# Optimization experiments

Measured on AMD Instinct MI355X. Metric: run time of the kernel, lower is better.

## Reference

```python
import jax, jax.numpy as jnp
import numpy as np

N = 50000          # node_num
E = 800000         # edges before self-loops (avg degree 16)
H = 1              # heads
C = 64             # out_channel (== embedding dim)
D_IN = 64          # in_channel
NEG_SLOPE = 0.2    # GraphLayer leaky_relu negative_slope
BN_EPS = 1e-5


def setup_inputs() -> dict:
    key = jax.random.key(0)
    ks = jax.random.split(key, 12)
    x = jax.random.normal(ks[0], (N, D_IN), jnp.float32)
    # random edges with no self-loops (forward removes then re-adds self-loops)
    src = jax.random.randint(ks[1], (E,), 0, N, dtype=jnp.int32)
    off = jax.random.randint(ks[2], (E,), 1, N, dtype=jnp.int32)
    dst = (src + off) % N
    edge_index = jnp.stack([src, dst])            # [2, E], row0=j (source), row1=i (target)
    embedding = jax.random.normal(ks[3], (N, C), jnp.float32)
    sc = 1.0 / np.sqrt(D_IN)
    W = jax.random.normal(ks[4], (H * C, D_IN), jnp.float32) * sc   # lin.weight
    att_i = jax.random.normal(ks[5], (1, H, C), jnp.float32) * 0.1
    att_j = jax.random.normal(ks[6], (1, H, C), jnp.float32) * 0.1
    att_em_i = jax.random.normal(ks[7], (1, H, C), jnp.float32) * 0.1
    att_em_j = jax.random.normal(ks[8], (1, H, C), jnp.float32) * 0.1
    bias = jnp.zeros((C,), jnp.float32)           # GraphLayer bias (concat=False)
    bn_gamma = jnp.ones((C,), jnp.float32)
    bn_beta = jnp.zeros((C,), jnp.float32)
    return {"x": x, "edge_index": edge_index, "embedding": embedding, "W": W,
            "att_i": att_i, "att_j": att_j, "att_em_i": att_em_i, "att_em_j": att_em_j,
            "bias": bias, "bn_gamma": bn_gamma, "bn_beta": bn_beta}


def reference(x, edge_index, embedding, W, att_i, att_j, att_em_i, att_em_j, bias, bn_gamma, bn_beta):
    n = x.shape[0]
    xl = (x @ W.T).reshape(n, H, C)                       # lin(x) -> [N, H, C]
    # add self-loops (input edges have none)
    loops = jnp.arange(n, dtype=edge_index.dtype)
    src = jnp.concatenate([edge_index[0], loops])         # j
    dst = jnp.concatenate([edge_index[1], loops])         # i (aggregation target)
    x_j = xl[src]                                         # [E', H, C]
    x_i = xl[dst]
    emb_i = embedding[dst][:, None, :]                    # [E', 1, C] broadcast over heads
    emb_j = embedding[src][:, None, :]
    # alpha = <cat(x_i, emb_i), cat(att_i, att_em_i)> + <cat(x_j, emb_j), cat(att_j, att_em_j)>
    a = ((x_i * att_i).sum(-1) + (emb_i * att_em_i).sum(-1)
         + (x_j * att_j).sum(-1) + (emb_j * att_em_j).sum(-1))   # [E', H]
    a = jnp.where(a >= 0, a, NEG_SLOPE * a)               # leaky_relu(0.2)
    # segment softmax over target nodes
    amax = jax.ops.segment_max(a, dst, num_segments=n)    # every node has a self-loop
    ea = jnp.exp(a - amax[dst])
    denom = jax.ops.segment_sum(ea, dst, num_segments=n)
    alpha = ea / (denom[dst] + 1e-16)                     # [E', H]
    msg = x_j * alpha[..., None]                          # [E', H, C]
    out = jax.ops.segment_sum(msg, dst, num_segments=n)   # [N, H, C]
    out = out.mean(axis=1) + bias                         # concat=False -> head mean
    # BatchNorm1d (training mode: batch stats) + ReLU
    mu = out.mean(axis=0)
    var = ((out - mu) ** 2).mean(axis=0)
    out = (out - mu) * jax.lax.rsqrt(var + BN_EPS) * bn_gamma + bn_beta
    return jnp.maximum(out, 0.0)
```

## Files before the change

kernel.cpp:

```cpp
#include <hip/hip_runtime.h>
#include <hip/hip_bf16.h>

#define NEG_SLOPE 0.2f
#define BN_EPS 1e-5f
#define CAP 48
#define OWNMAX 768

typedef __attribute__((ext_vector_type(8))) short bf16x8;
typedef __attribute__((ext_vector_type(4))) float f32x4;

__device__ __forceinline__ bf16x8 pk8(float4 a, float4 b) {
    union { __hip_bfloat16 h; short s; } u;
    bf16x8 r;
    u.h = __float2bfloat16(a.x); r[0] = u.s;
    u.h = __float2bfloat16(a.y); r[1] = u.s;
    u.h = __float2bfloat16(a.z); r[2] = u.s;
    u.h = __float2bfloat16(a.w); r[3] = u.s;
    u.h = __float2bfloat16(b.x); r[4] = u.s;
    u.h = __float2bfloat16(b.y); r[5] = u.s;
    u.h = __float2bfloat16(b.z); r[6] = u.s;
    u.h = __float2bfloat16(b.w); r[7] = u.s;
    return r;
}

__global__ void __launch_bounds__(256, 8)
k_scatter_mfma(const float* __restrict__ x, const float* __restrict__ W,
               const float* __restrict__ emb,
               const float* __restrict__ att_i, const float* __restrict__ att_j,
               const float* __restrict__ att_em_i, const float* __restrict__ att_em_j,
               const int* __restrict__ src, const int* __restrict__ dst, int E,
               int* __restrict__ cursor, unsigned short* __restrict__ bucket,
               __hip_bfloat16* __restrict__ xlh, float* __restrict__ s_i,
               float* __restrict__ s_j, int N) {
    __shared__ int nown;
    __shared__ unsigned int own[OWNMAX];
    int tid = threadIdx.x;

    int gw = blockIdx.x * 4 + (tid >> 6);
    int ntiles = (N + 15) >> 4;
    int lane = tid & 63;
    int m = lane & 15;
    int q = lane >> 4;
    int r0 = gw * 16;
    int rload = r0 + m; if (rload > N - 1) rload = N - 1;
    const float* xrow = x + (size_t)rload * 64;
    float4 xa0 = *(const float4*)(xrow + q * 8);
    float4 xa1 = *(const float4*)(xrow + q * 8 + 4);
    float4 xb0 = *(const float4*)(xrow + 32 + q * 8);
    float4 xb1 = *(const float4*)(xrow + 32 + q * 8 + 4);

    {
        int myx = blockIdx.x & 7;
        int slice = blockIdx.x >> 3;
        int per = ((E + 255) >> 8);
        per = (per + 3) & ~3;
        int e0 = slice * per;
        int e1 = e0 + per; if (e1 > E) e1 = E;
        if (tid == 0) nown = 0;
        __syncthreads();
        if (e0 < e1) {
            int e1a = e0 + ((e1 - e0) & ~3);
#define APP(dd, ss) if ((((dd) >> 6) & 7) == myx) { \
            int k_ = atomicAdd(&nown, 1); \
            if (k_ < OWNMAX) own[k_] = ((unsigned)(dd) << 16) | (unsigned)(ss); }
            for (int e = e0 + tid * 4; e < e1a; e += 1024) {
                int4 d4 = *(const int4*)(dst + e);
                int4 s4 = *(const int4*)(src + e);
                APP(d4.x, s4.x)
                APP(d4.y, s4.y)
                APP(d4.z, s4.z)
                APP(d4.w, s4.w)
            }
            for (int e = e1a + tid; e < e1; e += 256) {
                int d = dst[e]; int s = src[e];
                APP(d, s)
            }
#undef APP
        }
        __syncthreads();
        int n = nown < OWNMAX ? nown : OWNMAX;
        unsigned pa = (tid < n) ? own[tid] : 0u;
        unsigned pb = (tid + 256 < n) ? own[tid + 256] : 0u;
        if (tid < n) {
            int d = pa >> 16;
            int p = atomicAdd(&cursor[d], 1);
            if (p < CAP) bucket[(size_t)d * CAP + p] = (unsigned short)(pa & 0xffffu);
        }
        if (tid + 256 < n) {
            int d = pb >> 16;
            int p = atomicAdd(&cursor[d], 1);
            if (p < CAP) bucket[(size_t)d * CAP + p] = (unsigned short)(pb & 0xffffu);
        }
        for (int k = tid + 512; k < n; k += 256) {
            unsigned pc = own[k];
            int d = pc >> 16;
            int p = atomicAdd(&cursor[d], 1);
            if (p < CAP) bucket[(size_t)d * CAP + p] = (unsigned short)(pc & 0xffffu);
        }
    }

    if (gw >= ntiles) return;
    bf16x8 A0 = pk8(xa0, xa1);
    bf16x8 A1 = pk8(xb0, xb1);

    f32x4 acc0 = {0.f, 0.f, 0.f, 0.f}, acc1 = acc0, acc2 = acc0, acc3 = acc0;
#define CTILE(ct, accv) { \
        const float* wrow = W + (size_t)(ct * 16 + m) * 64; \
        float4 wb0 = *(const float4*)(wrow + q * 8); \
        float4 wb1 = *(const float4*)(wrow + q * 8 + 4); \
        float4 wb2 = *(const float4*)(wrow + 32 + q * 8); \
        float4 wb3 = *(const float4*)(wrow + 32 + q * 8 + 4); \
        bf16x8 B0 = pk8(wb0, wb1); \
        bf16x8 B1 = pk8(wb2, wb3); \
        accv = __builtin_amdgcn_mfma_f32_16x16x32_bf16(A0, B0, accv, 0, 0, 0); \
        accv = __builtin_amdgcn_mfma_f32_16x16x32_bf16(A1, B1, accv, 0, 0, 0); }
    CTILE(0, acc0) CTILE(1, acc1) CTILE(2, acc2) CTILE(3, acc3)
#undef CTILE

    float ati0 = att_i[m],    ati1 = att_i[16 + m],    ati2 = att_i[32 + m],    ati3 = att_i[48 + m];
    float atj0 = att_j[m],    atj1 = att_j[16 + m],    atj2 = att_j[32 + m],    atj3 = att_j[48 + m];
    float aei0 = att_em_i[m], aei1 = att_em_i[16 + m], aei2 = att_em_i[32 + m], aei3 = att_em_i[48 + m];
    float aej0 = att_em_j[m], aej1 = att_em_j[16 + m], aej2 = att_em_j[32 + m], aej3 = att_em_j[48 + m];
#pragma unroll
    for (int reg = 0; reg < 4; ++reg) {
        int r = r0 + q * 4 + reg;
        if (r < N) {
            float v0 = acc0[reg], v1 = acc1[reg], v2 = acc2[reg], v3 = acc3[reg];
            __hip_bfloat16* xo = xlh + (size_t)r * 64 + m;
            xo[0]  = __float2bfloat16(v0);
            xo[16] = __float2bfloat16(v1);
            xo[32] = __float2bfloat16(v2);
            xo[48] = __float2bfloat16(v3);
            const float* er = emb + (size_t)r * 64 + m;
            float e0 = er[0], e1 = er[16], e2 = er[32], e3 = er[48];
            float pi = v0 * ati0 + v1 * ati1 + v2 * ati2 + v3 * ati3
                     + e0 * aei0 + e1 * aei1 + e2 * aei2 + e3 * aei3;
            float pj = v0 * atj0 + v1 * atj1 + v2 * atj2 + v3 * atj3
                     + e0 * aej0 + e1 * aej1 + e2 * aej2 + e3 * aej3;
#pragma unroll
            for (int o = 1; o < 16; o <<= 1) {
                pi += __shfl_xor(pi, o, 64);
                pj += __shfl_xor(pj, o, 64);
            }
            if (m == 0) { s_i[r] = pi; s_j[r] = pj; }
        }
    }
}

__global__ void __launch_bounds__(256, 8)
k_aggregate(const __hip_bfloat16* __restrict__ xlh, const float* __restrict__ s_i,
            const float* __restrict__ s_j, const int* __restrict__ cursor,
            const unsigned short* __restrict__ bucket, const float* __restrict__ bias,
            __hip_bfloat16* __restrict__ preh, int N) {
    int lane = threadIdx.x & 63;
    int w = threadIdx.x >> 6;
    int blk = blockIdx.x;
    int t = blk >> 3;
    int g = ((t >> 4) << 7) + ((blk & 7) << 4) + (t & 15);
    int i = g * 4 + w;
    if (i >= N) return;

    int deg = cursor[i];
    deg = deg < CAP ? deg : CAP;
    size_t base = (size_t)i * CAP;
    float sii = s_i[i];
    float sji = s_j[i];
    float selfx = (float)xlh[(size_t)i * 64 + lane];
    float bi = bias[lane];
    int jreg = 0;
    if (lane < deg) jreg = (int)bucket[base + lane];
    float wreg = 0.f;
    if (lane < deg) {
        float a = sii + s_j[jreg];
        a = a >= 0.f ? a : NEG_SLOPE * a;
        wreg = __expf(a);
    }
    float a_self = sii + sji;
    a_self = a_self >= 0.f ? a_self : NEG_SLOPE * a_self;
    float w_self = __expf(a_self);
    float dsum = wreg;
#pragma unroll
    for (int o = 32; o; o >>= 1) dsum += __shfl_xor(dsum, o, 64);

    float acc = w_self * selfx;
    int wbits = __float_as_int(wreg);
    int nb = (deg + 15) >> 4;
#define GL(k) int j##k = __builtin_amdgcn_readlane(jreg, e + k); \
              float u##k = __int_as_float(__builtin_amdgcn_readlane(wbits, e + k)); \
              float v##k = (float)xlh[(size_t)j##k * 64 + lane];
#define FM(k) acc = fmaf(u##k, v##k, acc);
    for (int b = 0; b < nb; ++b) {
        int e = b << 4;
        GL(0) GL(1) GL(2) GL(3) GL(4) GL(5) GL(6) GL(7)
        GL(8) GL(9) GL(10) GL(11) GL(12) GL(13) GL(14) GL(15)
        FM(0) FM(1) FM(2) FM(3) FM(4) FM(5) FM(6) FM(7)
        FM(8) FM(9) FM(10) FM(11) FM(12) FM(13) FM(14) FM(15)
    }
#undef GL
#undef FM
    float denom = dsum + w_self + 1e-16f;
    preh[(size_t)i * 64 + lane] = __float2bfloat16(acc / denom + bi);
}

__global__ void k_stats(const __hip_bfloat16* __restrict__ preh, int N,
                        float* __restrict__ sums) {
    int lane = threadIdx.x & 63, w = threadIdx.x >> 6;
    int gwave = blockIdx.x * (blockDim.x >> 6) + w;
    int stride = gridDim.x * (blockDim.x >> 6);
    float s = 0.f, q = 0.f;
    for (int r = gwave; r < N; r += stride) {
        float v = (float)preh[(size_t)r * 64 + lane];
        s += v;
        q = fmaf(v, v, q);
    }
    __shared__ float ls[4][64], lq[4][64];
    ls[w][lane] = s;
    lq[w][lane] = q;
    __syncthreads();
    if (w == 0) {
        s = ls[0][lane] + ls[1][lane] + ls[2][lane] + ls[3][lane];
        q = lq[0][lane] + lq[1][lane] + lq[2][lane] + lq[3][lane];
        atomicAdd(&sums[lane], s);
        atomicAdd(&sums[64 + lane], q);
    }
}

__global__ void __launch_bounds__(256, 4)
k_norm(const __hip_bfloat16* __restrict__ preh, const float* __restrict__ sums,
       const float* __restrict__ gamma, const float* __restrict__ beta,
       float* __restrict__ out, int N, int total4) {
    __shared__ float sc_sh[64], sh_sh[64];
    int tid = threadIdx.x;
    if (tid < 64) {
        float invN = 1.f / (float)N;
        float mu = sums[tid] * invN;
        float var = sums[64 + tid] * invN - mu * mu;
        float sc = gamma[tid] * rsqrtf(var + BN_EPS);
        sc_sh[tid] = sc;
        sh_sh[tid] = beta[tid] - mu * sc;
    }
    __syncthreads();
    typedef __attribute__((ext_vector_type(4))) short s16x4;
    union { s16x4 v; short s[4]; } u;
    for (int i = blockIdx.x * blockDim.x + tid; i < total4; i += gridDim.x * blockDim.x) {
        int c = (i & 15) * 4;
        u.v = ((const s16x4*)preh)[i];
        float4 r;
        union { __hip_bfloat16 h; short s; } cv;
        cv.s = u.s[0]; r.x = fmaxf(fmaf((float)cv.h, sc_sh[c + 0], sh_sh[c + 0]), 0.f);
        cv.s = u.s[1]; r.y = fmaxf(fmaf((float)cv.h, sc_sh[c + 1], sh_sh[c + 1]), 0.f);
        cv.s = u.s[2]; r.z = fmaxf(fmaf((float)cv.h, sc_sh[c + 2], sh_sh[c + 2]), 0.f);
        cv.s = u.s[3]; r.w = fmaxf(fmaf((float)cv.h, sc_sh[c + 3], sh_sh[c + 3]), 0.f);
        ((float4*)out)[i] = r;
    }
}

extern "C" void kernel_launch(void* const* d_in, const int* in_sizes, int n_in,
                              void* d_out, int out_size, void* d_ws, size_t ws_size,
                              hipStream_t stream) {
    const float* x        = (const float*)d_in[0];
    const int*   ei       = (const int*)d_in[1];
    const float* emb      = (const float*)d_in[2];
    const float* W        = (const float*)d_in[3];
    const float* att_i    = (const float*)d_in[4];
    const float* att_j    = (const float*)d_in[5];
    const float* att_em_i = (const float*)d_in[6];
    const float* att_em_j = (const float*)d_in[7];
    const float* bias     = (const float*)d_in[8];
    const float* gamma    = (const float*)d_in[9];
    const float* beta     = (const float*)d_in[10];

    int N = in_sizes[0] / 64;
    int E = in_sizes[1] / 2;
    const int* srcv = ei;
    const int* dstv = ei + E;

    char* ws = (char*)d_ws;
    size_t o = 0;
    auto alloc = [&](size_t bytes) -> char* {
        char* p = ws + o;
        o += bytes;
        o = (o + 255) & ~(size_t)255;
        return p;
    };
    __hip_bfloat16* xlh    = (__hip_bfloat16*)alloc((size_t)N * 64 * 2);
    __hip_bfloat16* preh   = (__hip_bfloat16*)alloc((size_t)N * 64 * 2);
    float* s_i             = (float*)alloc((size_t)N * 4);
    float* s_j             = (float*)alloc((size_t)N * 4);
    unsigned short* bucket = (unsigned short*)alloc((size_t)N * CAP * 2);
    char*  zbase  = alloc((size_t)N * 4 + 128 * 4);
    int*   cursor = (int*)zbase;
    float* sums   = (float*)(zbase + (size_t)N * 4);

    hipMemsetAsync(zbase, 0, (size_t)N * 4 + 128 * 4, stream);

    k_scatter_mfma<<<2048, 256, 0, stream>>>(x, W, emb, att_i, att_j, att_em_i,
                                             att_em_j, srcv, dstv, E, cursor, bucket,
                                             xlh, s_i, s_j, N);
    int nblk2 = (((N + 3) / 4) + 127) & ~127;
    k_aggregate<<<nblk2, 256, 0, stream>>>(xlh, s_i, s_j, cursor, bucket,
                                           bias, preh, N);
    k_stats<<<256, 256, 0, stream>>>(preh, N, sums);
    int total4 = N * 16;
    k_norm<<<512, 256, 0, stream>>>(preh, sums, gamma, beta, (float*)d_out, N, total4);
}
```

Before: 180.0 us.

## Pair edges per wave in aggregation, remap GEMM tiles, add nontemporal loads/stores

The aggregation kernel now splits the wave into two half-waves that each gather a different neighbor row with 32-bit loads of two bf16 channels, then combines the halves with a cross-lane shuffle. This halves the number of serialized gather iterations per node. The fused scatter/GEMM kernel maps GEMM tiles across waves with a 2048-block stride and skips loading x for waves with no tile. Nontemporal hints are added on streaming loads and stores (x, emb, xlh writes, bucket, output) to reduce cache pollution. The changes add shuffle and select overhead, and the GEMM remap assumes a fixed grid size.

```diff
diff --git a/kernel.cpp b/kernel.cpp
--- a/kernel.cpp
+++ b/kernel.cpp
@@ -8,18 +8,19 @@
 
 typedef __attribute__((ext_vector_type(8))) short bf16x8;
 typedef __attribute__((ext_vector_type(4))) float f32x4;
-
-__device__ __forceinline__ bf16x8 pk8(float4 a, float4 b) {
+typedef __attribute__((ext_vector_type(4))) int i32x4;
+
+__device__ __forceinline__ bf16x8 pk8(f32x4 a, f32x4 b) {
     union { __hip_bfloat16 h; short s; } u;
     bf16x8 r;
-    u.h = __float2bfloat16(a.x); r[0] = u.s;
-    u.h = __float2bfloat16(a.y); r[1] = u.s;
-    u.h = __float2bfloat16(a.z); r[2] = u.s;
-    u.h = __float2bfloat16(a.w); r[3] = u.s;
-    u.h = __float2bfloat16(b.x); r[4] = u.s;
-    u.h = __float2bfloat16(b.y); r[5] = u.s;
-    u.h = __float2bfloat16(b.z); r[6] = u.s;
-    u.h = __float2bfloat16(b.w); r[7] = u.s;
+    u.h = __float2bfloat16(a[0]); r[0] = u.s;
+    u.h = __float2bfloat16(a[1]); r[1] = u.s;
+    u.h = __float2bfloat16(a[2]); r[2] = u.s;
+    u.h = __float2bfloat16(a[3]); r[3] = u.s;
+    u.h = __float2bfloat16(b[0]); r[4] = u.s;
+    u.h = __float2bfloat16(b[1]); r[5] = u.s;
+    u.h = __float2bfloat16(b[2]); r[6] = u.s;
+    u.h = __float2bfloat16(b[3]); r[7] = u.s;
     return r;
 }
 
@@ -35,19 +36,23 @@
     __shared__ int nown;
     __shared__ unsigned int own[OWNMAX];
     int tid = threadIdx.x;
-
-    int gw = blockIdx.x * 4 + (tid >> 6);
-    int ntiles = (N + 15) >> 4;
     int lane = tid & 63;
+    int wid = tid >> 6;
     int m = lane & 15;
     int q = lane >> 4;
+
+    int gw = wid * 2048 + (int)blockIdx.x;
+    int ntiles = (N + 15) >> 4;
+    bool hasgemm = gw < ntiles;
     int r0 = gw * 16;
-    int rload = r0 + m; if (rload > N - 1) rload = N - 1;
-    const float* xrow = x + (size_t)rload * 64;
-    float4 xa0 = *(const float4*)(xrow + q * 8);
-    float4 xa1 = *(const float4*)(xrow + q * 8 + 4);
-    float4 xb0 = *(const float4*)(xrow + 32 + q * 8);
-    float4 xb1 = *(const float4*)(xrow + 32 + q * 8 + 4);
+    f32x4 xa0 = {0,0,0,0}, xa1 = xa0, xb0 = xa0, xb1 = xa0;
+    if (hasgemm) {
+        const float* xrow = x + (size_t)(r0 + m) * 64;
+        xa0 = __builtin_nontemporal_load((const f32x4*)(xrow + q * 8));
+        xa1 = __builtin_nontemporal_load((const f32x4*)(xrow + q * 8 + 4));
+        xb0 = __builtin_nontemporal_load((const f32x4*)(xrow + 32 + q * 8));
+        xb1 = __builtin_nontemporal_load((const f32x4*)(xrow + 32 + q * 8 + 4));
+    }
 
     {
         int myx = blockIdx.x & 7;
@@ -64,12 +69,12 @@
             int k_ = atomicAdd(&nown, 1); \
             if (k_ < OWNMAX) own[k_] = ((unsigned)(dd) << 16) | (unsigned)(ss); }
             for (int e = e0 + tid * 4; e < e1a; e += 1024) {
-                int4 d4 = *(const int4*)(dst + e);
-                int4 s4 = *(const int4*)(src + e);
-                APP(d4.x, s4.x)
-                APP(d4.y, s4.y)
-                APP(d4.z, s4.z)
-                APP(d4.w, s4.w)
+                i32x4 d4 = *(const i32x4*)(dst + e);
+                i32x4 s4 = *(const i32x4*)(src + e);
+                APP(d4[0], s4[0])
+                APP(d4[1], s4[1])
+                APP(d4[2], s4[2])
+                APP(d4[3], s4[3])
             }
             for (int e = e1a + tid; e < e1; e += 256) {
                 int d = dst[e]; int s = src[e];
@@ -99,17 +104,17 @@
         }
     }
 
-    if (gw >= ntiles) return;
+    if (!hasgemm) return;
     bf16x8 A0 = pk8(xa0, xa1);
     bf16x8 A1 = pk8(xb0, xb1);
 
     f32x4 acc0 = {0.f, 0.f, 0.f, 0.f}, acc1 = acc0, acc2 = acc0, acc3 = acc0;
 #define CTILE(ct, accv) { \
         const float* wrow = W + (size_t)(ct * 16 + m) * 64; \
-        float4 wb0 = *(const float4*)(wrow + q * 8); \
-        float4 wb1 = *(const float4*)(wrow + q * 8 + 4); \
-        float4 wb2 = *(const float4*)(wrow + 32 + q * 8); \
-        float4 wb3 = *(const float4*)(wrow + 32 + q * 8 + 4); \
+        f32x4 wb0 = *(const f32x4*)(wrow + q * 8); \
+        f32x4 wb1 = *(const f32x4*)(wrow + q * 8 + 4); \
+        f32x4 wb2 = *(const f32x4*)(wrow + 32 + q * 8); \
+        f32x4 wb3 = *(const f32x4*)(wrow + 32 + q * 8 + 4); \
         bf16x8 B0 = pk8(wb0, wb1); \
         bf16x8 B1 = pk8(wb2, wb3); \
         accv = __builtin_amdgcn_mfma_f32_16x16x32_bf16(A0, B0, accv, 0, 0, 0); \
@@ -121,18 +126,22 @@
     float atj0 = att_j[m],    atj1 = att_j[16 + m],    atj2 = att_j[32 + m],    atj3 = att_j[48 + m];
     float aei0 = att_em_i[m], aei1 = att_em_i[16 + m], aei2 = att_em_i[32 + m], aei3 = att_em_i[48 + m];
     float aej0 = att_em_j[m], aej1 = att_em_j[16 + m], aej2 = att_em_j[32 + m], aej3 = att_em_j[48 + m];
+    union { __hip_bfloat16 h; short s; } cv;
 #pragma unroll
     for (int reg = 0; reg < 4; ++reg) {
         int r = r0 + q * 4 + reg;
         if (r < N) {
             float v0 = acc0[reg], v1 = acc1[reg], v2 = acc2[reg], v3 = acc3[reg];
-            __hip_bfloat16* xo = xlh + (size_t)r * 64 + m;
-            xo[0]  = __float2bfloat16(v0);
-            xo[16] = __float2bfloat16(v1);
-            xo[32] = __float2bfloat16(v2);
-            xo[48] = __float2bfloat16(v3);
+            short* xo = (short*)xlh + (size_t)r * 64 + m;
+            cv.h = __float2bfloat16(v0); __builtin_nontemporal_store(cv.s, xo);
+            cv.h = __float2bfloat16(v1); __builtin_nontemporal_store(cv.s, xo + 16);
+            cv.h = __float2bfloat16(v2); __builtin_nontemporal_store(cv.s, xo + 32);
+            cv.h = __float2bfloat16(v3); __builtin_nontemporal_store(cv.s, xo + 48);
             const float* er = emb + (size_t)r * 64 + m;
-            float e0 = er[0], e1 = er[16], e2 = er[32], e3 = er[48];
+            float e0 = __builtin_nontemporal_load(er);
+            float e1 = __builtin_nontemporal_load(er + 16);
+            float e2 = __builtin_nontemporal_load(er + 32);
+            float e3 = __builtin_nontemporal_load(er + 48);
             float pi = v0 * ati0 + v1 * ati1 + v2 * ati2 + v3 * ati3
                      + e0 * aei0 + e1 * aei1 + e2 * aei2 + e3 * aei3;
             float pj = v0 * atj0 + v1 * atj1 + v2 * atj2 + v3 * atj3
@@ -165,10 +174,13 @@
     size_t base = (size_t)i * CAP;
     float sii = s_i[i];
     float sji = s_j[i];
-    float selfx = (float)xlh[(size_t)i * 64 + lane];
-    float bi = bias[lane];
+    int half = lane >> 5;
+    int cl = lane & 31;
+    unsigned selfp = *(const unsigned*)((const char*)xlh + ((size_t)i << 7) + (cl << 2));
+    float bi0 = bias[2 * cl], bi1 = bias[2 * cl + 1];
+
     int jreg = 0;
-    if (lane < deg) jreg = (int)bucket[base + lane];
+    if (lane < deg) jreg = (int)__builtin_nontemporal_load(bucket + base + lane);
     float wreg = 0.f;
     if (lane < deg) {
         float a = sii + s_j[jreg];
@@ -182,24 +194,41 @@
 #pragma unroll
     for (int o = 32; o; o >>= 1) dsum += __shfl_xor(dsum, o, 64);
 
-    float acc = w_self * selfx;
+    union { __hip_bfloat16 h; short s; } cu;
+    cu.s = (short)(selfp & 0xffffu);  float sx0 = (float)cu.h;
+    cu.s = (short)(selfp >> 16);      float sx1 = (float)cu.h;
+    float ws0 = half ? 0.f : w_self;
+    float acc0 = ws0 * sx0;
+    float acc1 = ws0 * sx1;
     int wbits = __float_as_int(wreg);
-    int nb = (deg + 15) >> 4;
-#define GL(k) int j##k = __builtin_amdgcn_readlane(jreg, e + k); \
-              float u##k = __int_as_float(__builtin_amdgcn_readlane(wbits, e + k)); \
-              float v##k = (float)xlh[(size_t)j##k * 64 + lane];
-#define FM(k) acc = fmaf(u##k, v##k, acc);
-    for (int b = 0; b < nb; ++b) {
-        int e = b << 4;
-        GL(0) GL(1) GL(2) GL(3) GL(4) GL(5) GL(6) GL(7)
-        GL(8) GL(9) GL(10) GL(11) GL(12) GL(13) GL(14) GL(15)
-        FM(0) FM(1) FM(2) FM(3) FM(4) FM(5) FM(6) FM(7)
-        FM(8) FM(9) FM(10) FM(11) FM(12) FM(13) FM(14) FM(15)
-    }
-#undef GL
-#undef FM
+    int np = (deg + 1) >> 1;
+#define GLP(k) int jA##k = __builtin_amdgcn_readlane(jreg, 2*(p0+k)); \
+               int jB##k = __builtin_amdgcn_readlane(jreg, 2*(p0+k)+1); \
+               float uA##k = __int_as_float(__builtin_amdgcn_readlane(wbits, 2*(p0+k))); \
+               float uB##k = __int_as_float(__builtin_amdgcn_readlane(wbits, 2*(p0+k)+1)); \
+               int jme##k = half ? jB##k : jA##k; \
+               unsigned pv##k = *(const unsigned*)((const char*)xlh + ((size_t)jme##k << 7) + (cl << 2));
+#define FMP(k) { float um = half ? uB##k : uA##k; \
+               cu.s = (short)(pv##k & 0xffffu); acc0 = fmaf(um, (float)cu.h, acc0); \
+               cu.s = (short)(pv##k >> 16);     acc1 = fmaf(um, (float)cu.h, acc1); }
+    for (int p0 = 0; p0 < np; p0 += 4) {
+        GLP(0) GLP(1) GLP(2) GLP(3)
+        FMP(0) FMP(1) FMP(2) FMP(3)
+    }
+#undef GLP
+#undef FMP
+    acc0 += __shfl_xor(acc0, 32, 64);
+    acc1 += __shfl_xor(acc1, 32, 64);
     float denom = dsum + w_self + 1e-16f;
-    preh[(size_t)i * 64 + lane] = __float2bfloat16(acc / denom + bi);
+    float r0 = acc0 / denom + bi0;
+    float r1 = acc1 / denom + bi1;
+    if (lane < 32) {
+        union { __hip_bfloat16 h; unsigned short s; } h0, h1;
+        h0.h = __float2bfloat16(r0);
+        h1.h = __float2bfloat16(r1);
+        unsigned pv = (unsigned)h0.s | ((unsigned)h1.s << 16);
+        *((unsigned*)preh + (size_t)i * 32 + cl) = pv;
+    }
 }
 
 __global__ void k_stats(const __hip_bfloat16* __restrict__ preh, int N,
@@ -245,13 +274,13 @@
     for (int i = blockIdx.x * blockDim.x + tid; i < total4; i += gridDim.x * blockDim.x) {
         int c = (i & 15) * 4;
         u.v = ((const s16x4*)preh)[i];
-        float4 r;
+        f32x4 r;
         union { __hip_bfloat16 h; short s; } cv;
-        cv.s = u.s[0]; r.x = fmaxf(fmaf((float)cv.h, sc_sh[c + 0], sh_sh[c + 0]), 0.f);
-        cv.s = u.s[1]; r.y = fmaxf(fmaf((float)cv.h, sc_sh[c + 1], sh_sh[c + 1]), 0.f);
-        cv.s = u.s[2]; r.z = fmaxf(fmaf((float)cv.h, sc_sh[c + 2], sh_sh[c + 2]), 0.f);
-        cv.s = u.s[3]; r.w = fmaxf(fmaf((float)cv.h, sc_sh[c + 3], sh_sh[c + 3]), 0.f);
-        ((float4*)out)[i] = r;
+        cv.s = u.s[0]; r[0] = fmaxf(fmaf((float)cv.h, sc_sh[c + 0], sh_sh[c + 0]), 0.f);
+        cv.s = u.s[1]; r[1] = fmaxf(fmaf((float)cv.h, sc_sh[c + 1], sh_sh[c + 1]), 0.f);
+        cv.s = u.s[2]; r[2] = fmaxf(fmaf((float)cv.h, sc_sh[c + 2], sh_sh[c + 2]), 0.f);
+        cv.s = u.s[3]; r[3] = fmaxf(fmaf((float)cv.h, sc_sh[c + 3], sh_sh[c + 3]), 0.f);
+        __builtin_nontemporal_store(r, (f32x4*)out + i);
     }
 }
 
```

After: 191.2 us. +6.2%, slower.
